# Kernel tuning notes

Hardware: AMD Instinct MI355X
Metric: run time of the kernel (lower is better)

Reference implementation:

```python
import jax, jax.numpy as jnp
import numpy as np

EPS = 1e-9

def setup_inputs() -> dict:
    key = jax.random.key(0)
    k1, k2, k3, k4 = jax.random.split(key, 4)
    B, D, M, R, C = 1024, 16, 4, 4096, 64
    x = jax.random.normal(k1, (B, D), dtype=jnp.float32)
    centers = jax.random.normal(k2, (D, M), dtype=jnp.float32)
    widths = jnp.ones((D, M), dtype=jnp.float32)
    consequents = jax.random.normal(k3, (R, D + 1, C), dtype=jnp.float32)
    rules = jax.random.randint(k4, (R, D), 0, M)  # rule -> MF index per input dim
    return {"x": x, "centers": centers, "widths": widths,
            "consequents": consequents, "rules": rules}

def reference(x, centers, widths, consequents, rules):
    B, D = x.shape
    # Gaussian membership values: [B, D, M]
    mfs = jnp.exp(-(x[:, :, None] - centers[None]) ** 2 / (2.0 * widths[None] ** 2)) + EPS
    # Gather per-rule MFs: rule_mfs[b, d, r] = mfs[b, d, rules[r, d]] -> [B, D, R]
    rule_mfs = jnp.take_along_axis(mfs, rules.T[None, :, :], axis=2)
    # Product firing strengths and normalization: [B, R]
    fs = jnp.prod(rule_mfs, axis=1)
    nfs = fs / (fs.sum(axis=1, keepdims=True) + EPS)
    # Extended input with bias: [B, D+1]
    x_ext = jnp.concatenate([x, jnp.ones((B, 1), dtype=x.dtype)], axis=1)
    # NOTE: faithful to the original torch code: 'bi,rjc->brc' has no shared
    # contraction index, so it sums x_ext over i and consequents over j.
    rule_out = jnp.einsum('br,brc->bc', nfs,
                          jnp.einsum('bi,rjc->brc', x_ext, consequents))
    return rule_out, nfs, x_ext
```

## Files before the change

kernel.cpp:

```cpp
#include <hip/hip_runtime.h>
#include <hip/hip_bf16.h>

typedef __attribute__((ext_vector_type(8))) short short8;
typedef __attribute__((ext_vector_type(4))) short short4v;
typedef __attribute__((ext_vector_type(4))) float floatx4;
typedef __attribute__((ext_vector_type(4))) unsigned int uintx4;
typedef unsigned int u32;
typedef unsigned short u16;

#define NB 1024
#define ND 16
#define NM 4
#define NR 4096
#define NC 64
#define EPSF 1e-9f
#define KSPLIT 8

__device__ inline u16 f2bf(float f) {
    u32 u;
    __builtin_memcpy(&u, &f, 4);
    u32 lsb = (u >> 16) & 1;
    u += 0x7fffu + lsb;
    return (u16)(u >> 16);
}

__global__ __launch_bounds__(256) void k_prep(const float* __restrict__ cons,
                                              const int* __restrict__ rules,
                                              u16* __restrict__ s_consT,
                                              u32* __restrict__ packed) {
    __shared__ u16 tile[16][68];
    int rbase = blockIdx.x * 16;
    int tid = threadIdx.x;
    int c = tid & 63;
    {
        int rr = tid >> 6;
#pragma unroll
        for (int it = 0; it < 4; ++it, rr += 4) {
            const float* p = cons + (size_t)(rbase + rr) * (ND + 1) * NC + c;
            float s = 0.f;
#pragma unroll
            for (int j = 0; j < ND + 1; ++j) s += p[j * NC];
            tile[rr][c] = f2bf(s);
        }
    }
    if (tid < 16) {
        const int* q = rules + (size_t)(rbase + tid) * ND;
        u32 pk = 0;
#pragma unroll
        for (int d = 0; d < ND; ++d) pk |= ((u32)(q[d] & 3)) << (2 * d);
        packed[rbase + tid] = pk;
    }
    __syncthreads();
    {
        int cc = tid >> 2;
        int r0 = (tid & 3) * 4;
        short4v v;
#pragma unroll
        for (int e = 0; e < 4; ++e) v[e] = (short)tile[r0 + e][cc];
        *(short4v*)(s_consT + (size_t)cc * NR + rbase + r0) = v;
    }
}

__global__ __launch_bounds__(256) void k_fs(const float* __restrict__ x,
                                            const float* __restrict__ centers,
                                            const float* __restrict__ widths,
                                            const u32* __restrict__ packed,
                                            float* __restrict__ out_nfs,
                                            u16* __restrict__ nfs_bf,
                                            float* __restrict__ out_xe,
                                            float* __restrict__ sx) {
    __shared__ float xv[16];
    __shared__ float mftab[64];
    __shared__ float gtab[1024];
    __shared__ float fsbuf[4096];
    __shared__ float wred[4];
    __shared__ float s_inv;
    int b = blockIdx.x;
    int tid = threadIdx.x;
    if (tid < 16) {
        float raw = x[b * 16 + tid];
        xv[tid] = raw;
        out_xe[b * 17 + tid] = raw;
    }
    if (tid == 16) out_xe[b * 17 + 16] = 1.0f;
    __syncthreads();
    if (tid < 64) {
        float diff = xv[tid >> 2] - centers[tid];
        float w = widths[tid];
        mftab[tid] = __expf(-diff * diff / (2.f * w * w)) + EPSF;
    }
    if (tid == 0) {
        float s = 1.f;
        for (int i = 0; i < 16; ++i) s += xv[i];
        sx[b] = s;
    }
    __syncthreads();
    for (int idx = tid; idx < 1024; idx += 256) {
        int g = idx >> 8, i = idx & 255;
        const float* mf = mftab + g * 16;
        gtab[idx] = mf[0 + (i & 3)] * mf[4 + ((i >> 2) & 3)] *
                    mf[8 + ((i >> 4) & 3)] * mf[12 + ((i >> 6) & 3)];
    }
    __syncthreads();
    float lsum = 0.f;
#pragma unroll
    for (int it = 0; it < 4; ++it) {
        int r = it * 1024 + tid * 4;
        uintx4 p = *(const uintx4*)(packed + r);
        floatx4 f;
#pragma unroll
        for (int e = 0; e < 4; ++e) {
            u32 pk = p[e];
            f[e] = gtab[pk & 255] * gtab[256 + ((pk >> 8) & 255)] *
                   gtab[512 + ((pk >> 16) & 255)] * gtab[768 + (pk >> 24)];
            lsum += f[e];
        }
        *(floatx4*)(fsbuf + r) = f;
    }
    for (int off = 32; off; off >>= 1) lsum += __shfl_down(lsum, off, 64);
    if ((tid & 63) == 0) wred[tid >> 6] = lsum;
    __syncthreads();
    if (tid == 0) s_inv = 1.f / (wred[0] + wred[1] + wred[2] + wred[3] + EPSF);
    __syncthreads();
    float inv = s_inv;
    float* on = out_nfs + (size_t)b * NR;
    u16* ob = nfs_bf + (size_t)b * NR;
#pragma unroll
    for (int it = 0; it < 4; ++it) {
        int r = it * 1024 + tid * 4;
        floatx4 f = *(const floatx4*)(fsbuf + r);
        floatx4 v;
        short4v bv;
#pragma unroll
        for (int e = 0; e < 4; ++e) {
            v[e] = f[e] * inv;
            bv[e] = (short)f2bf(v[e]);
        }
        *(floatx4*)(on + r) = v;
        *(short4v*)(ob + r) = bv;
    }
}

__global__ __launch_bounds__(256) void k_gemm(const u16* __restrict__ nfs,
                                              const u16* __restrict__ s_consT,
                                              float* __restrict__ part) {
    int rt = blockIdx.x;
    int ks = blockIdx.y;
    int tid = threadIdx.x;
    int wid = tid >> 6, lane = tid & 63;
    int arow = rt * 64 + wid * 16 + (lane & 15);
    int klane = (lane >> 4) * 8;
    int kbase = ks * (NR / KSPLIT);
    const u16* aptr = nfs + (size_t)arow * NR + kbase + klane;
    const u16* bptr = s_consT + (size_t)(lane & 15) * NR + kbase + klane;
    floatx4 acc[4] = {};
#pragma unroll 4
    for (int t = 0; t < 16; ++t) {
        short8 af = *(const short8*)(aptr + t * 32);
#pragma unroll
        for (int cb = 0; cb < 4; ++cb) {
            short8 bf = *(const short8*)(bptr + (size_t)cb * 16 * NR + t * 32);
            acc[cb] = __builtin_amdgcn_mfma_f32_16x16x32_bf16(af, bf, acc[cb], 0, 0, 0);
        }
    }
    float* po = part + (size_t)ks * (NB * NC);
#pragma unroll
    for (int cb = 0; cb < 4; ++cb)
#pragma unroll
        for (int reg = 0; reg < 4; ++reg) {
            int row = rt * 64 + wid * 16 + (lane >> 4) * 4 + reg;
            int col = cb * 16 + (lane & 15);
            po[(size_t)row * NC + col] = acc[cb][reg];
        }
}

__global__ __launch_bounds__(256) void k_out(const float* __restrict__ part,
                                             const float* __restrict__ sx,
                                             float* __restrict__ out0) {
    int t = blockIdx.x * 256 + threadIdx.x;
    if (t >= NB * NC) return;
    float a = 0.f;
#pragma unroll
    for (int ks = 0; ks < KSPLIT; ++ks) a += part[(size_t)ks * (NB * NC) + t];
    out0[t] = a * sx[t >> 6];
}

extern "C" void kernel_launch(void* const* d_in, const int* in_sizes, int n_in,
                              void* d_out, int out_size, void* d_ws, size_t ws_size,
                              hipStream_t stream) {
    const float* x = (const float*)d_in[0];
    const float* centers = (const float*)d_in[1];
    const float* widths = (const float*)d_in[2];
    const float* cons = (const float*)d_in[3];
    const int* rules = (const int*)d_in[4];

    float* out = (float*)d_out;
    float* out_rule = out;
    float* out_nfs = out + NB * NC;
    float* out_xe = out + NB * NC + NB * NR;

    char* ws = (char*)d_ws;
    u16* s_consT = (u16*)ws;
    u32* packed = (u32*)(ws + (512 << 10));
    float* sx = (float*)(ws + (512 << 10) + (16 << 10));
    float* part = (float*)(ws + (512 << 10) + (20 << 10));
    u16* nfs_bf = (u16*)(ws + (512 << 10) + (20 << 10) + (NB * NC * KSPLIT * 4));

    k_prep<<<NR / 16, 256, 0, stream>>>(cons, rules, s_consT, packed);
    k_fs<<<NB, 256, 0, stream>>>(x, centers, widths, packed, out_nfs, nfs_bf, out_xe, sx);
    k_gemm<<<dim3(NB / 64, KSPLIT), 256, 0, stream>>>(nfs_bf, s_consT, part);
    k_out<<<(NB * NC + 255) / 256, 256, 0, stream>>>(part, sx, out_rule);
}
```

Before: 33.34 us.

## Fuse split-K reduction into GEMM via atomics and drop bf16 nfs copy

Removes the separate bf16 copy of normalized firing strengths. The GEMM now reads the fp32 nfs output directly and converts it to bf16 in registers. The split-K partial buffer and the final reduction kernel are replaced by atomicAdd into the output, which is zeroed in the prep kernel and scaled by sx inside the GEMM. KSPLIT is doubled, and k_fs keeps firing strengths in registers instead of a 16KB shared buffer. This removes one launch and the partial-buffer traffic, but the GEMM reads twice the A bytes, contends on atomics, and accumulates in a non-deterministic order.

```diff
diff --git a/kernel.cpp b/kernel.cpp
--- a/kernel.cpp
+++ b/kernel.cpp
@@ -14,7 +14,7 @@
 #define NR 4096
 #define NC 64
 #define EPSF 1e-9f
-#define KSPLIT 8
+#define KSPLIT 16
 
 __device__ inline u16 f2bf(float f) {
     u32 u;
@@ -27,11 +27,13 @@
 __global__ __launch_bounds__(256) void k_prep(const float* __restrict__ cons,
                                               const int* __restrict__ rules,
                                               u16* __restrict__ s_consT,
-                                              u32* __restrict__ packed) {
+                                              u32* __restrict__ packed,
+                                              float* __restrict__ out_rule) {
     __shared__ u16 tile[16][68];
     int rbase = blockIdx.x * 16;
     int tid = threadIdx.x;
     int c = tid & 63;
+    out_rule[blockIdx.x * 256 + tid] = 0.f;
     {
         int rr = tid >> 6;
 #pragma unroll
@@ -66,13 +68,11 @@
                                             const float* __restrict__ widths,
                                             const u32* __restrict__ packed,
                                             float* __restrict__ out_nfs,
-                                            u16* __restrict__ nfs_bf,
                                             float* __restrict__ out_xe,
                                             float* __restrict__ sx) {
     __shared__ float xv[16];
     __shared__ float mftab[64];
     __shared__ float gtab[1024];
-    __shared__ float fsbuf[4096];
     __shared__ float wred[4];
     __shared__ float s_inv;
     int b = blockIdx.x;
@@ -102,20 +102,19 @@
                     mf[8 + ((i >> 4) & 3)] * mf[12 + ((i >> 6) & 3)];
     }
     __syncthreads();
+    floatx4 f[4];
     float lsum = 0.f;
 #pragma unroll
     for (int it = 0; it < 4; ++it) {
         int r = it * 1024 + tid * 4;
         uintx4 p = *(const uintx4*)(packed + r);
-        floatx4 f;
 #pragma unroll
         for (int e = 0; e < 4; ++e) {
             u32 pk = p[e];
-            f[e] = gtab[pk & 255] * gtab[256 + ((pk >> 8) & 255)] *
-                   gtab[512 + ((pk >> 16) & 255)] * gtab[768 + (pk >> 24)];
-            lsum += f[e];
-        }
-        *(floatx4*)(fsbuf + r) = f;
+            f[it][e] = gtab[pk & 255] * gtab[256 + ((pk >> 8) & 255)] *
+                       gtab[512 + ((pk >> 16) & 255)] * gtab[768 + (pk >> 24)];
+            lsum += f[it][e];
+        }
     }
     for (int off = 32; off; off >>= 1) lsum += __shfl_down(lsum, off, 64);
     if ((tid & 63) == 0) wred[tid >> 6] = lsum;
@@ -124,65 +123,56 @@
     __syncthreads();
     float inv = s_inv;
     float* on = out_nfs + (size_t)b * NR;
-    u16* ob = nfs_bf + (size_t)b * NR;
 #pragma unroll
     for (int it = 0; it < 4; ++it) {
         int r = it * 1024 + tid * 4;
-        floatx4 f = *(const floatx4*)(fsbuf + r);
         floatx4 v;
-        short4v bv;
-#pragma unroll
-        for (int e = 0; e < 4; ++e) {
-            v[e] = f[e] * inv;
-            bv[e] = (short)f2bf(v[e]);
-        }
+#pragma unroll
+        for (int e = 0; e < 4; ++e) v[e] = f[it][e] * inv;
         *(floatx4*)(on + r) = v;
-        *(short4v*)(ob + r) = bv;
-    }
-}
-
-__global__ __launch_bounds__(256) void k_gemm(const u16* __restrict__ nfs,
+    }
+}
+
+__global__ __launch_bounds__(256) void k_gemm(const float* __restrict__ nfs,
                                               const u16* __restrict__ s_consT,
-                                              float* __restrict__ part) {
+                                              const float* __restrict__ sx,
+                                              float* __restrict__ out_rule) {
     int rt = blockIdx.x;
     int ks = blockIdx.y;
     int tid = threadIdx.x;
     int wid = tid >> 6, lane = tid & 63;
     int arow = rt * 64 + wid * 16 + (lane & 15);
-    int klane = (lane >> 4) * 8;
-    int kbase = ks * (NR / KSPLIT);
-    const u16* aptr = nfs + (size_t)arow * NR + kbase + klane;
-    const u16* bptr = s_consT + (size_t)(lane & 15) * NR + kbase + klane;
+    int kbase = ks * (NR / KSPLIT) + (lane >> 4) * 8;
+    const float* aptr = nfs + (size_t)arow * NR + kbase;
+    const u16* bptr = s_consT + (size_t)(lane & 15) * NR + kbase;
     floatx4 acc[4] = {};
-#pragma unroll 4
-    for (int t = 0; t < 16; ++t) {
-        short8 af = *(const short8*)(aptr + t * 32);
+#pragma unroll
+    for (int t = 0; t < (NR / KSPLIT) / 32; ++t) {
+        floatx4 alo = *(const floatx4*)(aptr + t * 32);
+        floatx4 ahi = *(const floatx4*)(aptr + t * 32 + 4);
+        short8 af;
+#pragma unroll
+        for (int e = 0; e < 4; ++e) {
+            af[e] = (short)f2bf(alo[e]);
+            af[e + 4] = (short)f2bf(ahi[e]);
+        }
 #pragma unroll
         for (int cb = 0; cb < 4; ++cb) {
             short8 bf = *(const short8*)(bptr + (size_t)cb * 16 * NR + t * 32);
             acc[cb] = __builtin_amdgcn_mfma_f32_16x16x32_bf16(af, bf, acc[cb], 0, 0, 0);
         }
     }
-    float* po = part + (size_t)ks * (NB * NC);
+    int orow0 = rt * 64 + wid * 16 + (lane >> 4) * 4;
+    float s4[4];
+#pragma unroll
+    for (int reg = 0; reg < 4; ++reg) s4[reg] = sx[orow0 + reg];
 #pragma unroll
     for (int cb = 0; cb < 4; ++cb)
 #pragma unroll
         for (int reg = 0; reg < 4; ++reg) {
-            int row = rt * 64 + wid * 16 + (lane >> 4) * 4 + reg;
             int col = cb * 16 + (lane & 15);
-            po[(size_t)row * NC + col] = acc[cb][reg];
-        }
-}
-
-__global__ __launch_bounds__(256) void k_out(const float* __restrict__ part,
-                                             const float* __restrict__ sx,
-                                             float* __restrict__ out0) {
-    int t = blockIdx.x * 256 + threadIdx.x;
-    if (t >= NB * NC) return;
-    float a = 0.f;
-#pragma unroll
-    for (int ks = 0; ks < KSPLIT; ++ks) a += part[(size_t)ks * (NB * NC) + t];
-    out0[t] = a * sx[t >> 6];
+            atomicAdd(out_rule + (size_t)(orow0 + reg) * NC + col, acc[cb][reg] * s4[reg]);
+        }
 }
 
 extern "C" void kernel_launch(void* const* d_in, const int* in_sizes, int n_in,
@@ -203,11 +193,8 @@
     u16* s_consT = (u16*)ws;
     u32* packed = (u32*)(ws + (512 << 10));
     float* sx = (float*)(ws + (512 << 10) + (16 << 10));
-    float* part = (float*)(ws + (512 << 10) + (20 << 10));
-    u16* nfs_bf = (u16*)(ws + (512 << 10) + (20 << 10) + (NB * NC * KSPLIT * 4));
-
-    k_prep<<<NR / 16, 256, 0, stream>>>(cons, rules, s_consT, packed);
-    k_fs<<<NB, 256, 0, stream>>>(x, centers, widths, packed, out_nfs, nfs_bf, out_xe, sx);
-    k_gemm<<<dim3(NB / 64, KSPLIT), 256, 0, stream>>>(nfs_bf, s_consT, part);
-    k_out<<<(NB * NC + 255) / 256, 256, 0, stream>>>(part, sx, out_rule);
-}
+
+    k_prep<<<NR / 16, 256, 0, stream>>>(cons, rules, s_consT, packed, out_rule);
+    k_fs<<<NB, 256, 0, stream>>>(x, centers, widths, packed, out_nfs, out_xe, sx);
+    k_gemm<<<dim3(16, KSPLIT), 256, 0, stream>>>(out_nfs, s_consT, sx, out_rule);
+}
```

New measurement: 32.02 us. 4.0% less time.
